# Optimization experiments

Measured on AMD Instinct MI355X. Metric: run time of the kernel, lower is better.

The kernel has to match this reference:

```python
import jax, jax.numpy as jnp
import numpy as np
from jax import lax

K_LOCAL = 8
CHUNK = 1024


def _local_features(template, surf_xyz, point_feat):
    # template: (B,T,3), surf_xyz: (B,S,3), point_feat: (B,S,D)
    B, T, _ = template.shape
    _, S, D = point_feat.shape
    n_chunks = T // CHUNK  # T chosen divisible by CHUNK
    tmpl = template.reshape(B, n_chunks, CHUNK, 3).transpose(1, 0, 2, 3)  # (n_chunks,B,c,3)
    s_sq = jnp.sum(surf_xyz * surf_xyz, axis=-1)  # (B,S)

    def body(carry, t):  # t: (B,c,3)
        t_sq = jnp.sum(t * t, axis=-1)  # (B,c)
        # squared distances; monotone in true distance so top-k indices match cdist
        d2 = t_sq[..., None] + s_sq[:, None, :] - 2.0 * jnp.einsum('bcd,bsd->bcs', t, surf_xyz)
        _, idx = lax.top_k(-d2, K_LOCAL)  # (B,c,k) nearest
        flat = idx.reshape(B, -1)  # (B,c*k)
        g = jnp.take_along_axis(point_feat, flat[..., None], axis=1)  # (B,c*k,D)
        local = g.reshape(B, CHUNK, K_LOCAL, D).mean(axis=2)  # (B,c,D)
        return carry, local

    _, locals_ = lax.scan(body, None, tmpl)  # (n_chunks,B,c,D)
    return locals_.transpose(1, 0, 2, 3).reshape(B, T, D)


def setup_inputs() -> dict:
    key = jax.random.key(0)
    ks = jax.random.split(key, 12)
    B, T, S, D, G = 4, 16384, 8192, 256, 512
    inp_dim, H = 3 + D + G, 256
    w = lambda k, sh: (jax.random.normal(k, sh, dtype=jnp.float32) * 0.02)
    return {
        'template': jax.random.normal(ks[0], (B, T, 3), dtype=jnp.float32),
        'surf_xyz': jax.random.normal(ks[1], (B, S, 3), dtype=jnp.float32),
        'global_feat': jax.random.normal(ks[2], (B, G), dtype=jnp.float32),
        'point_feat': jax.random.normal(ks[3], (B, S, D), dtype=jnp.float32),
        'dw1': w(ks[4], (inp_dim, H)), 'db1': jnp.zeros((H,), jnp.float32),
        'dw2': w(ks[5], (H, H)), 'db2': jnp.zeros((H,), jnp.float32),
        'dw3': w(ks[6], (H, 3)), 'db3': jnp.zeros((3,), jnp.float32),
        'mw1': w(ks[7], (inp_dim, H // 2)), 'mb1': jnp.zeros((H // 2,), jnp.float32),
        'mw2': w(ks[8], (H // 2, 64)), 'mb2': jnp.zeros((64,), jnp.float32),
        'mw3': w(ks[9], (64, 1)), 'mb3': jnp.zeros((1,), jnp.float32),
    }


def reference(template, surf_xyz, global_feat, point_feat,
              dw1, db1, dw2, db2, dw3, db3,
              mw1, mb1, mw2, mb2, mw3, mb3):
    B, T, _ = template.shape
    local = _local_features(template, surf_xyz, point_feat)  # (B,T,256)
    g = jnp.broadcast_to(global_feat[:, None, :], (B, T, global_feat.shape[-1]))
    x = jnp.concatenate([template, local, g], axis=-1)  # (B,T,771)
    # disp head (dropout = identity in eval)
    h = jax.nn.relu(x @ dw1 + db1)
    h = jax.nn.relu(h @ dw2 + db2)
    disp = h @ dw3 + db3  # (B,T,3)
    # material head
    m = jax.nn.relu(x @ mw1 + mb1)
    m = jax.nn.relu(m @ mw2 + mb2)
    mat = jax.nn.sigmoid(m @ mw3 + mb3)[..., 0]  # (B,T)
    return disp, mat
```

## Files before the change

### kernel.cpp

```cpp
#include <hip/hip_runtime.h>
#include <cstdint>


#define T_PTS 16384
#define S_PTS 8192
#define B_SZ 4
#define D_FEAT 256
#define G_FEAT 512
#define M_ROWS (B_SZ * T_PTS)
#define K1 320
#define N1 384
#define DISP_SZ (M_ROWS * 3)
#define NCHUNK 2
#define CHUNK_S (S_PTS / NCHUNK)
#define NPLANE (NCHUNK * 8)
#define NCELL 32768

using u16 = unsigned short;
typedef short bf16x8 __attribute__((ext_vector_type(8)));
typedef float f32x4 __attribute__((ext_vector_type(4)));

__device__ __forceinline__ u16 f2bf(float f) {
  uint32_t x = __builtin_bit_cast(uint32_t, f);
  x += 0x7fffu + ((x >> 16) & 1u);
  return (u16)(x >> 16);
}
__device__ __forceinline__ float bf2f(u16 h) {
  uint32_t x = ((uint32_t)h) << 16;
  return __builtin_bit_cast(float, x);
}
__device__ __forceinline__ void gload16(void* lds, const void* g) {
  __builtin_amdgcn_global_load_lds(
      (const __attribute__((address_space(1))) unsigned int*)g,
      (__attribute__((address_space(3))) unsigned int*)lds, 16, 0, 0);
}


__global__ __launch_bounds__(256) void prep_surf(const float* __restrict__ sxyz,
                                                 float4* __restrict__ surfp) {
  int i = blockIdx.x * 256 + threadIdx.x;
  float x = sxyz[(size_t)i * 3], y = sxyz[(size_t)i * 3 + 1], z = sxyz[(size_t)i * 3 + 2];
  float4 v;
  v.x = x; v.y = y; v.z = z; v.w = fmaf(x, x, fmaf(y, y, z * z));
  surfp[i] = v;
}

__global__ __launch_bounds__(256) void prep_w(
    const float* __restrict__ dw1, const float* __restrict__ mw1,
    const float* __restrict__ dw2, const float* __restrict__ mw2,
    u16* __restrict__ w1t, u16* __restrict__ w2t, u16* __restrict__ w2bt) {
  int i = blockIdx.x * 256 + threadIdx.x;
  if (i < 122880) {
    int n = i / 320, k = i % 320;
    float v = 0.f;
    if (k < 256)      v = (n < 256) ? dw1[(size_t)(3 + k) * 256 + n] : mw1[(size_t)(3 + k) * 128 + (n - 256)];
    else if (k < 259) v = (n < 256) ? dw1[(size_t)(k - 256) * 256 + n] : mw1[(size_t)(k - 256) * 128 + (n - 256)];
    w1t[i] = f2bf(v);
  } else if (i < 188416) {
    int j = i - 122880;
    int n = j >> 8, k = j & 255;
    w2t[j] = f2bf(dw2[(size_t)k * 256 + n]);
  } else {
    int j = i - 188416;
    int n = j >> 7, k = j & 127;
    w2bt[j] = f2bf(mw2[(size_t)k * 64 + n]);
  }
}

__global__ __launch_bounds__(512) void bias1_k(
    const float* __restrict__ gf, const float* __restrict__ dw1,
    const float* __restrict__ mw1, const float* __restrict__ db1,
    const float* __restrict__ mb1, float* __restrict__ bias1) {
  __shared__ float red[512];
  int b = blockIdx.x, nc = blockIdx.y;
  int tn = threadIdx.x & 127, tk = threadIdx.x >> 7;
  int n = nc * 128 + tn;
  const float* g = gf + b * G_FEAT;
  float s = 0.f;
  if (n < 256) {
    for (int k = tk * 128; k < tk * 128 + 128; k++)
      s = fmaf(g[k], dw1[(size_t)(259 + k) * 256 + n], s);
  } else {
    for (int k = tk * 128; k < tk * 128 + 128; k++)
      s = fmaf(g[k], mw1[(size_t)(259 + k) * 128 + (n - 256)], s);
  }
  red[threadIdx.x] = s;
  __syncthreads();
  if (tk == 0) {
    float base = (n < 256) ? db1[n] : mb1[n - 256];
    bias1[b * N1 + n] = base + ((red[tn] + red[tn + 128]) + (red[tn + 256] + red[tn + 384]));
  }
}


__device__ __forceinline__ int spread5(int v) {
  return (v & 1) | ((v & 2) << 2) | ((v & 4) << 4) | ((v & 8) << 6) | ((v & 16) << 8);
}
__device__ __forceinline__ int morton15(float x, float y, float z) {
  int ix = (int)fminf(31.f, fmaxf(0.f, (x + 4.f) * 4.f));
  int iy = (int)fminf(31.f, fmaxf(0.f, (y + 4.f) * 4.f));
  int iz = (int)fminf(31.f, fmaxf(0.f, (z + 4.f) * 4.f));
  return (spread5(ix) << 2) | (spread5(iy) << 1) | spread5(iz);
}

__global__ __launch_bounds__(256) void zbins_k(int* __restrict__ bins) {
  bins[blockIdx.x * 256 + threadIdx.x] = 0;
}

__global__ __launch_bounds__(256) void hist_t_k(const float* __restrict__ tmpl,
                                                int* __restrict__ bins_t,
                                                int* __restrict__ cellb) {
  int i = blockIdx.x * 256 + threadIdx.x;
  int b = i >> 14;
  int c = morton15(tmpl[(size_t)i * 3], tmpl[(size_t)i * 3 + 1], tmpl[(size_t)i * 3 + 2]);
  cellb[i] = c;
  atomicAdd(&bins_t[b * NCELL + c], 1);
}

__global__ __launch_bounds__(1024) void scan_k(int* __restrict__ bins) {
  __shared__ int sd[2048];
  int* bb = bins + blockIdx.x * NCELL;
  int tid = threadIdx.x;
  int running = 0;
  for (int c = 0; c < NCELL / 1024; ++c) {
    int v = bb[c * 1024 + tid];
    sd[tid] = v;
    __syncthreads();
    int cur = 0;
#pragma unroll
    for (int s = 0; s < 10; ++s) {
      int off = 1 << s;
      int val = sd[cur * 1024 + tid] + ((tid >= off) ? sd[cur * 1024 + tid - off] : 0);
      sd[(1 - cur) * 1024 + tid] = val;
      __syncthreads();
      cur ^= 1;
    }
    int incl = sd[cur * 1024 + tid];
    bb[c * 1024 + tid] = running + incl - v;
    running += sd[cur * 1024 + 1023];
    __syncthreads();
  }
}

__global__ __launch_bounds__(256) void scatter_t_k(const float* __restrict__ tmpl,
                                                   const int* __restrict__ cellb,
                                                   int* __restrict__ bins_t,
                                                   int* __restrict__ perm,
                                                   float4* __restrict__ tmplS) {
  int i = blockIdx.x * 256 + threadIdx.x;
  int b = i >> 14, t = i & 16383;
  int pos = atomicAdd(&bins_t[b * NCELL + cellb[i]], 1);
  int dst = (b << 14) + pos;
  perm[dst] = t;
  float4 v;
  v.x = tmpl[(size_t)i * 3]; v.y = tmpl[(size_t)i * 3 + 1]; v.z = tmpl[(size_t)i * 3 + 2];
  v.w = 0.f;
  tmplS[dst] = v;
}

__global__ __launch_bounds__(256) void knn_part_k(const float4* __restrict__ surfp,
                                                  const float4* __restrict__ tmplS,
                                                  float* __restrict__ part_d,
                                                  int* __restrict__ part_i) {
  const int ch = blockIdx.y, b = blockIdx.z;
  const int t = (blockIdx.x << 8) + threadIdx.x;
  const int gi = b * T_PTS + t;

  const float4* sp = surfp + (size_t)b * S_PTS + ch * CHUNK_S;

  float4 tp = tmplS[gi];
  float nx = -2.f * tp.x, ny = -2.f * tp.y, nz = -2.f * tp.z;
  float tsq = fmaf(tp.x, tp.x, fmaf(tp.y, tp.y, tp.z * tp.z));

  float dd[8]; int ii[8];
#pragma unroll
  for (int q = 0; q < 8; q++) { dd[q] = 3e38f; ii[q] = 0; }
  float worst = 3e38f;

  auto proc = [&](const float4* c, int base) {
    float d2[8];
#pragma unroll
    for (int q = 0; q < 8; q++)
      d2[q] = fmaf(nx, c[q].x, fmaf(ny, c[q].y, fmaf(nz, c[q].z, tsq + c[q].w)));
    float m = fminf(fminf(fminf(d2[0], d2[1]), fminf(d2[2], d2[3])),
                    fminf(fminf(d2[4], d2[5]), fminf(d2[6], d2[7])));
    while (m < worst) {
      int qi = 7;
#pragma unroll
      for (int q = 6; q >= 0; --q) qi = (d2[q] == m) ? q : qi;
      int gx = base + qi;
#pragma unroll
      for (int r = 7; r >= 1; --r) {
        bool cr = m < dd[r], cr1 = m < dd[r - 1];
        dd[r] = cr ? (cr1 ? dd[r - 1] : m) : dd[r];
        ii[r] = cr ? (cr1 ? ii[r - 1] : gx) : ii[r];
      }
      bool c0 = m < dd[0];
      dd[0] = c0 ? m : dd[0];
      ii[0] = c0 ? gx : ii[0];
      worst = dd[7];
#pragma unroll
      for (int q = 0; q < 8; ++q) d2[q] = (q == qi) ? 3e38f : d2[q];
      m = fminf(fminf(fminf(d2[0], d2[1]), fminf(d2[2], d2[3])),
                fminf(fminf(d2[4], d2[5]), fminf(d2[6], d2[7])));
    }
  };

  float4 ca[8], cb[8];
#pragma unroll
  for (int q = 0; q < 8; q++) ca[q] = sp[q];

  constexpr int NG = CHUNK_S / 8;
  for (int g = 0; g < NG; g += 2) {
#pragma unroll
    for (int q = 0; q < 8; q++) cb[q] = sp[(g + 1) * 8 + q];
    proc(ca, g * 8);
#pragma unroll
    for (int q = 0; q < 8; q++) ca[q] = sp[((g + 2) & (NG - 1)) * 8 + q];
    proc(cb, (g + 1) * 8);
  }

#pragma unroll
  for (int q = 0; q < 8; q++) {
    part_d[(size_t)(ch * 8 + q) * M_ROWS + gi] = dd[q];
    part_i[(size_t)(ch * 8 + q) * M_ROWS + gi] = ii[q] + ch * CHUNK_S;
  }
}

__global__ __launch_bounds__(256) void knn_merge_k(const float* __restrict__ part_d,
                                                   const int* __restrict__ part_i,
                                                   int* __restrict__ knn) {
  int pt = blockIdx.x * 256 + threadIdx.x;
  float d[NPLANE]; int x[NPLANE];
#pragma unroll
  for (int q = 0; q < NPLANE; q++) {
    d[q] = part_d[(size_t)q * M_ROWS + pt];
    x[q] = part_i[(size_t)q * M_ROWS + pt];
  }
#pragma unroll
  for (int s = 0; s < 8; s++) {
    float bd = d[0]; int bx = x[0]; int bp = 0;
#pragma unroll
    for (int q = 1; q < NPLANE; q++) {
      bool lt = (d[q] < bd) || (d[q] == bd && x[q] < bx);
      bd = lt ? d[q] : bd;
      bx = lt ? x[q] : bx;
      bp = lt ? q : bp;
    }
    knn[(size_t)pt * 8 + s] = bx;
#pragma unroll
    for (int q = 0; q < NPLANE; q++)
      if (q == bp) d[q] = 3e38f;
  }
}

__global__ __launch_bounds__(256) void gather_k(const int* __restrict__ knn,
                                                const float* __restrict__ pf,
                                                const float4* __restrict__ tmplS,
                                                u16* __restrict__ xb) {
  int m = blockIdx.x * 4 + (threadIdx.x >> 6);
  int lane = threadIdx.x & 63;
  int b = m >> 14;
  const int* id = knn + (size_t)m * 8;
  const float* base = pf + (size_t)b * S_PTS * D_FEAT;
  float ax = 0, ay = 0, az = 0, aw = 0;
#pragma unroll
  for (int k = 0; k < 8; k++) {
    const float4* p = (const float4*)(base + (size_t)id[k] * D_FEAT) + lane;
    float4 v = *p;
    ax += v.x; ay += v.y; az += v.z; aw += v.w;
  }
  ushort4 o;
  o.x = f2bf(ax * 0.125f); o.y = f2bf(ay * 0.125f);
  o.z = f2bf(az * 0.125f); o.w = f2bf(aw * 0.125f);
  *(ushort4*)(xb + (size_t)m * K1 + lane * 4) = o;
  float4 tp = tmplS[m];
  float tv = (lane == 0) ? tp.x : (lane == 1) ? tp.y : (lane == 2) ? tp.z : 0.f;
  xb[(size_t)m * K1 + 256 + lane] = f2bf(tv);
}

template <int BM, int BN>
__global__ __launch_bounds__(256) void gemm_k(const u16* __restrict__ X, int ldx,
                                              const u16* __restrict__ Wt,
                                              const float* __restrict__ bias, int bstride,
                                              u16* __restrict__ Y, int ldy, int K) {
  constexpr int WM = 2, WN = 2;
  constexpr int FM = BM / WM / 16, FN = BN / WN / 16;
  __shared__ u16 As[BM * 64];
  __shared__ u16 Bs[BN * 64];
  const int tid = threadIdx.x, lane = tid & 63, wid = tid >> 6;
  const int m0 = blockIdx.x * BM, n0 = blockIdx.y * BN;
  const int wm0 = (wid / WN) * (BM / WM), wn0 = (wid % WN) * (BN / WN);

  f32x4 acc[FM][FN] = {};

  for (int kt = 0; kt < K; kt += 64) {
#pragma unroll
    for (int i = 0; i < BM * 8 / 256; i++) {
      int c = i * 256 + tid;
      int r = c >> 3, s = c & 7;
      int ss = s ^ (r & 7);
      gload16(As + c * 8, X + (size_t)(m0 + r) * ldx + kt + ss * 8);
    }
#pragma unroll
    for (int i = 0; i < BN * 8 / 256; i++) {
      int c = i * 256 + tid;
      int r = c >> 3, s = c & 7;
      int ss = s ^ (r & 7);
      gload16(Bs + c * 8, Wt + (size_t)(n0 + r) * K + kt + ss * 8);
    }
    __syncthreads();
#pragma unroll
    for (int kk = 0; kk < 2; kk++) {
      bf16x8 af[FM], bfr[FN];
#pragma unroll
      for (int i = 0; i < FM; i++) {
        int r = wm0 + i * 16 + (lane & 15);
        int q = kk * 4 + (lane >> 4);
        af[i] = *(const bf16x8*)(As + r * 64 + ((q ^ (r & 7)) * 8));
      }
#pragma unroll
      for (int j = 0; j < FN; j++) {
        int r = wn0 + j * 16 + (lane & 15);
        int q = kk * 4 + (lane >> 4);
        bfr[j] = *(const bf16x8*)(Bs + r * 64 + ((q ^ (r & 7)) * 8));
      }
#pragma unroll
      for (int i = 0; i < FM; i++)
#pragma unroll
        for (int j = 0; j < FN; j++)
          acc[i][j] = __builtin_amdgcn_mfma_f32_16x16x32_bf16(af[i], bfr[j], acc[i][j], 0, 0, 0);
    }
    __syncthreads();
  }

  const float* brow = bias + (size_t)(m0 / T_PTS) * bstride;
#pragma unroll
  for (int i = 0; i < FM; i++)
#pragma unroll
    for (int j = 0; j < FN; j++)
#pragma unroll
      for (int r = 0; r < 4; r++) {
        int rl = wm0 + i * 16 + (lane >> 4) * 4 + r;
        int cl = wn0 + j * 16 + (lane & 15);
        float v = acc[i][j][r] + brow[n0 + cl];
        v = fmaxf(v, 0.f);
        Y[(size_t)(m0 + rl) * ldy + n0 + cl] = f2bf(v);
      }
}

__global__ __launch_bounds__(256) void final_k(const u16* __restrict__ h2,
                                               const u16* __restrict__ m2,
                                               const float* __restrict__ dw3,
                                               const float* __restrict__ db3,
                                               const float* __restrict__ mw3,
                                               const float* __restrict__ mb3,
                                               const int* __restrict__ perm,
                                               float* __restrict__ out) {
  int m = blockIdx.x * 4 + (threadIdx.x >> 6);
  int lane = threadIdx.x & 63;
  ushort4 hv = *(const ushort4*)(h2 + (size_t)m * 256 + lane * 4);
  float hq[4] = {bf2f(hv.x), bf2f(hv.y), bf2f(hv.z), bf2f(hv.w)};
  float a0 = 0, a1 = 0, a2 = 0, am = 0;
#pragma unroll
  for (int q = 0; q < 4; q++) {
    int k = lane * 4 + q;
    a0 = fmaf(hq[q], dw3[(size_t)k * 3 + 0], a0);
    a1 = fmaf(hq[q], dw3[(size_t)k * 3 + 1], a1);
    a2 = fmaf(hq[q], dw3[(size_t)k * 3 + 2], a2);
  }
  if (lane < 16) {
    ushort4 mv = *(const ushort4*)(m2 + (size_t)m * 64 + lane * 4);
    float mq[4] = {bf2f(mv.x), bf2f(mv.y), bf2f(mv.z), bf2f(mv.w)};
#pragma unroll
    for (int q = 0; q < 4; q++) am = fmaf(mq[q], mw3[lane * 4 + q], am);
  }
#pragma unroll
  for (int off = 32; off > 0; off >>= 1) {
    a0 += __shfl_down(a0, off);
    a1 += __shfl_down(a1, off);
    a2 += __shfl_down(a2, off);
    am += __shfl_down(am, off);
  }
  if (lane == 0) {
    int b = m >> 14;
    int orig = (b << 14) + perm[m];
    out[(size_t)orig * 3 + 0] = a0 + db3[0];
    out[(size_t)orig * 3 + 1] = a1 + db3[1];
    out[(size_t)orig * 3 + 2] = a2 + db3[2];
    float s = am + mb3[0];
    out[DISP_SZ + orig] = 1.f / (1.f + expf(-s));
  }
}


extern "C" void kernel_launch(void* const* d_in, const int* in_sizes, int n_in,
                              void* d_out, int out_size, void* d_ws, size_t ws_size,
                              hipStream_t stream) {
  const float* tmpl = (const float*)d_in[0];
  const float* sxyz = (const float*)d_in[1];
  const float* gf   = (const float*)d_in[2];
  const float* pf   = (const float*)d_in[3];
  const float* dw1  = (const float*)d_in[4];
  const float* db1  = (const float*)d_in[5];
  const float* dw2  = (const float*)d_in[6];
  const float* db2  = (const float*)d_in[7];
  const float* dw3  = (const float*)d_in[8];
  const float* db3  = (const float*)d_in[9];
  const float* mw1  = (const float*)d_in[10];
  const float* mb1  = (const float*)d_in[11];
  const float* mw2  = (const float*)d_in[12];
  const float* mb2  = (const float*)d_in[13];
  const float* mw3  = (const float*)d_in[14];
  const float* mb3  = (const float*)d_in[15];

  char* ws = (char*)d_ws;
  float4* surfp  = (float4*)(ws + 0);
  int*    knn    = (int*)(ws + 524288);
  u16*    xb     = (u16*)(ws + 2621440);
  float*  part_d = (float*)(ws + 2621440);
  int*    part_i = (int*)(ws + 11010048);
  u16*    w1t    = (u16*)(ws + 44564480);
  u16*    w2t    = (u16*)(ws + 44810240);
  u16*    w2bt   = (u16*)(ws + 44941312);
  float*  bias1  = (float*)(ws + 44957696);
  u16*    h1     = (u16*)(ws + 44963840);
  int*    cellb  = (int*)(ws + 44963840);
  int*    bins   = (int*)(ws + 45225984);
  float4* tmplS  = (float4*)(ws + 45750272);
  u16*    h2     = (u16*)(ws + 95295488);
  u16*    m2     = (u16*)(ws + 128849920);
  int*    perm   = (int*)(ws + 137238528);
  float*  out    = (float*)d_out;

  prep_surf<<<128, 256, 0, stream>>>(sxyz, surfp);
  prep_w<<<768, 256, 0, stream>>>(dw1, mw1, dw2, mw2, w1t, w2t, w2bt);
  bias1_k<<<dim3(B_SZ, 3), 512, 0, stream>>>(gf, dw1, mw1, db1, mb1, bias1);
  zbins_k<<<512, 256, 0, stream>>>(bins);
  hist_t_k<<<256, 256, 0, stream>>>(tmpl, bins, cellb);
  scan_k<<<B_SZ, 1024, 0, stream>>>(bins);
  scatter_t_k<<<256, 256, 0, stream>>>(tmpl, cellb, bins, perm, tmplS);
  knn_part_k<<<dim3(64, NCHUNK, B_SZ), 256, 0, stream>>>(surfp, tmplS, part_d, part_i);
  knn_merge_k<<<256, 256, 0, stream>>>(part_d, part_i, knn);
  gather_k<<<16384, 256, 0, stream>>>(knn, pf, tmplS, xb);
  gemm_k<128, 128><<<dim3(512, 3), 256, 0, stream>>>(xb, K1, w1t, bias1, N1, h1, N1, K1);
  gemm_k<128, 128><<<dim3(512, 2), 256, 0, stream>>>(h1, N1, w2t, db2, 0, h2, 256, 256);
  gemm_k<128, 64><<<dim3(512, 1), 256, 0, stream>>>(h1 + 256, N1, w2bt, mb2, 0, m2, 64, 128);
  final_k<<<16384, 256, 0, stream>>>(h2, m2, dw3, db3, mw3, mb3, perm, out);
}
```

Before: 518.3 us.

## Parallelize cell prefix scan, split KNN into more chunks, simplify insertion loop

Replaces the four-block serial prefix scan over 32768 Morton cells with a two-level scan: 64 blocks each scan 2048 cells, then a tiny kernel computes segment offsets that scatter adds to the per-cell positions. Doubles the number of surface chunks in the partial KNN so more blocks run in parallel, at the cost of more partial candidates for the merge step. Also replaces the extract-min loop in the top-8 insertion with a straight pass over the eight candidates that inserts any below the current worst.

```diff
diff --git a/kernel.cpp b/kernel.cpp
--- a/kernel.cpp
+++ b/kernel.cpp
@@ -11,7 +11,7 @@
 #define K1 320
 #define N1 384
 #define DISP_SZ (M_ROWS * 3)
-#define NCHUNK 2
+#define NCHUNK 4
 #define CHUNK_S (S_PTS / NCHUNK)
 #define NPLANE (NCHUNK * 8)
 #define NCELL 32768
@@ -117,40 +117,52 @@
   atomicAdd(&bins_t[b * NCELL + c], 1);
 }
 
-__global__ __launch_bounds__(1024) void scan_k(int* __restrict__ bins) {
+__global__ __launch_bounds__(1024) void scan1_k(int* __restrict__ bins,
+                                                int* __restrict__ segsum) {
   __shared__ int sd[2048];
-  int* bb = bins + blockIdx.x * NCELL;
+  int seg = blockIdx.x, tid = threadIdx.x;
+  int* bb = bins + seg * 2048;
+  int e0 = bb[2 * tid], e1 = bb[2 * tid + 1];
+  sd[tid] = e0 + e1;
+  __syncthreads();
+  int cur = 0;
+#pragma unroll
+  for (int s = 0; s < 10; ++s) {
+    int off = 1 << s;
+    int val = sd[cur * 1024 + tid] + ((tid >= off) ? sd[cur * 1024 + tid - off] : 0);
+    sd[(1 - cur) * 1024 + tid] = val;
+    __syncthreads();
+    cur ^= 1;
+  }
+  int incl = sd[cur * 1024 + tid];
+  int excl = incl - (e0 + e1);
+  bb[2 * tid] = excl;
+  bb[2 * tid + 1] = excl + e0;
+  if (tid == 1023) segsum[seg] = incl;
+}
+
+__global__ __launch_bounds__(64) void scan2_k(int* __restrict__ segsum) {
+  __shared__ int tot[64];
   int tid = threadIdx.x;
-  int running = 0;
-  for (int c = 0; c < NCELL / 1024; ++c) {
-    int v = bb[c * 1024 + tid];
-    sd[tid] = v;
-    __syncthreads();
-    int cur = 0;
-#pragma unroll
-    for (int s = 0; s < 10; ++s) {
-      int off = 1 << s;
-      int val = sd[cur * 1024 + tid] + ((tid >= off) ? sd[cur * 1024 + tid - off] : 0);
-      sd[(1 - cur) * 1024 + tid] = val;
-      __syncthreads();
-      cur ^= 1;
-    }
-    int incl = sd[cur * 1024 + tid];
-    bb[c * 1024 + tid] = running + incl - v;
-    running += sd[cur * 1024 + 1023];
-    __syncthreads();
-  }
+  int b = tid >> 4, w = tid & 15;
+  tot[tid] = segsum[tid];
+  __syncthreads();
+  int s = 0;
+  for (int j = 0; j < 16; ++j) s += (j < w) ? tot[b * 16 + j] : 0;
+  segsum[tid] = s;
 }
 
 __global__ __launch_bounds__(256) void scatter_t_k(const float* __restrict__ tmpl,
                                                    const int* __restrict__ cellb,
                                                    int* __restrict__ bins_t,
+                                                   const int* __restrict__ segbase,
                                                    int* __restrict__ perm,
                                                    float4* __restrict__ tmplS) {
   int i = blockIdx.x * 256 + threadIdx.x;
   int b = i >> 14, t = i & 16383;
-  int pos = atomicAdd(&bins_t[b * NCELL + cellb[i]], 1);
-  int dst = (b << 14) + pos;
+  int idx = b * NCELL + cellb[i];
+  int local = atomicAdd(&bins_t[idx], 1);
+  int dst = (b << 14) + segbase[idx >> 11] + local;
   perm[dst] = t;
   float4 v;
   v.x = tmpl[(size_t)i * 3]; v.y = tmpl[(size_t)i * 3 + 1]; v.z = tmpl[(size_t)i * 3 + 2];
@@ -184,25 +196,24 @@
       d2[q] = fmaf(nx, c[q].x, fmaf(ny, c[q].y, fmaf(nz, c[q].z, tsq + c[q].w)));
     float m = fminf(fminf(fminf(d2[0], d2[1]), fminf(d2[2], d2[3])),
                     fminf(fminf(d2[4], d2[5]), fminf(d2[6], d2[7])));
-    while (m < worst) {
-      int qi = 7;
-#pragma unroll
-      for (int q = 6; q >= 0; --q) qi = (d2[q] == m) ? q : qi;
-      int gx = base + qi;
-#pragma unroll
-      for (int r = 7; r >= 1; --r) {
-        bool cr = m < dd[r], cr1 = m < dd[r - 1];
-        dd[r] = cr ? (cr1 ? dd[r - 1] : m) : dd[r];
-        ii[r] = cr ? (cr1 ? ii[r - 1] : gx) : ii[r];
+    if (m < worst) {
+#pragma unroll
+      for (int q = 0; q < 8; ++q) {
+        float v = d2[q];
+        if (v < worst) {
+          int gx = base + q;
+#pragma unroll
+          for (int r = 7; r >= 1; --r) {
+            bool cr = v < dd[r], cr1 = v < dd[r - 1];
+            dd[r] = cr ? (cr1 ? dd[r - 1] : v) : dd[r];
+            ii[r] = cr ? (cr1 ? ii[r - 1] : gx) : ii[r];
+          }
+          bool c0 = v < dd[0];
+          dd[0] = c0 ? v : dd[0];
+          ii[0] = c0 ? gx : ii[0];
+          worst = dd[7];
+        }
       }
-      bool c0 = m < dd[0];
-      dd[0] = c0 ? m : dd[0];
-      ii[0] = c0 ? gx : ii[0];
-      worst = dd[7];
-#pragma unroll
-      for (int q = 0; q < 8; ++q) d2[q] = (q == qi) ? 3e38f : d2[q];
-      m = fminf(fminf(fminf(d2[0], d2[1]), fminf(d2[2], d2[3])),
-                fminf(fminf(d2[4], d2[5]), fminf(d2[6], d2[7])));
     }
   };
 
@@ -427,7 +438,8 @@
   u16*    h1     = (u16*)(ws + 44963840);
   int*    cellb  = (int*)(ws + 44963840);
   int*    bins   = (int*)(ws + 45225984);
-  float4* tmplS  = (float4*)(ws + 45750272);
+  int*    segsum = (int*)(ws + 45750272);
+  float4* tmplS  = (float4*)(ws + 45750528);
   u16*    h2     = (u16*)(ws + 95295488);
   u16*    m2     = (u16*)(ws + 128849920);
   int*    perm   = (int*)(ws + 137238528);
@@ -438,8 +450,9 @@
   bias1_k<<<dim3(B_SZ, 3), 512, 0, stream>>>(gf, dw1, mw1, db1, mb1, bias1);
   zbins_k<<<512, 256, 0, stream>>>(bins);
   hist_t_k<<<256, 256, 0, stream>>>(tmpl, bins, cellb);
-  scan_k<<<B_SZ, 1024, 0, stream>>>(bins);
-  scatter_t_k<<<256, 256, 0, stream>>>(tmpl, cellb, bins, perm, tmplS);
+  scan1_k<<<64, 1024, 0, stream>>>(bins, segsum);
+  scan2_k<<<1, 64, 0, stream>>>(segsum);
+  scatter_t_k<<<256, 256, 0, stream>>>(tmpl, cellb, bins, segsum, perm, tmplS);
   knn_part_k<<<dim3(64, NCHUNK, B_SZ), 256, 0, stream>>>(surfp, tmplS, part_d, part_i);
   knn_merge_k<<<256, 256, 0, stream>>>(part_d, part_i, knn);
   gather_k<<<16384, 256, 0, stream>>>(knn, pf, tmplS, xb);
```

Measured after the change: 423.9 us. 18.2% less time.
